# Optimization experiments

Measured on AMD Instinct MI355X. Metric: run time of the kernel, lower is better.

Reference implementation:

```python
import jax, jax.numpy as jnp
import numpy as np

B, M, N, L = 8, 384, 1536, 20  # batch, checks (detectors), error mechanisms, BP layers
ROW_W = 8  # check-node degree of sparse parity-check matrix H


def setup_inputs() -> dict:
    key = jax.random.key(0)
    ks = jax.random.split(key, 10)
    # Sparse binary check matrix: each row has exactly ROW_W ones (LDPC-like DEM).
    rng = np.random.default_rng(0)
    H_np = np.zeros((M, N), np.float32)
    for i in range(M):
        H_np[i, rng.choice(N, ROW_W, replace=False)] = 1.0
    H = jnp.asarray(H_np)
    llrs = jax.random.uniform(ks[0], (N,), minval=0.5, maxval=2.0)
    syndromes = jax.random.randint(ks[1], (B, M, 1), 0, 2).astype(jnp.float32)
    errors = jax.random.randint(ks[2], (B, N), 0, 2).astype(jnp.float32)
    # Per-layer learned weights (damped so 20 BP iterations stay numerically stable).
    weights_de = jax.random.uniform(ks[3], (L, M, N), minval=0.1, maxval=0.25)
    weights_llr = jax.random.uniform(ks[4], (L, N), minval=0.5, maxval=1.0)
    marg_weights_de = jax.random.uniform(ks[5], (M, N), minval=0.5, maxval=1.0)
    marg_weights_llr = jax.random.uniform(ks[6], (N,), minval=0.5, maxval=1.0)
    residual_weights = jax.random.uniform(ks[7], (L,), minval=0.0, maxval=0.1)
    rhos = jnp.ones((L,), jnp.float32) / L  # init: ones normalized by layers
    return dict(syndromes=syndromes, errors=errors, H=H, llrs=llrs,
                weights_de=weights_de, weights_llr=weights_llr,
                marg_weights_de=marg_weights_de, marg_weights_llr=marg_weights_llr,
                residual_weights=residual_weights, rhos=rhos)


def reference(syndromes, errors, H, llrs, weights_de, weights_llr,
              marg_weights_de, marg_weights_llr, residual_weights, rhos):
    sign = (1.0 - 2.0 * syndromes) * H          # (B,M,N): (-1)^syndrome masked by H
    one_minus_e = 1.0 - errors                  # (B,N)

    def step(msg_dn, per_layer):
        w_de, w_llr, res_w, rho = per_layer
        # --- error (variable) node update ---
        base = H * (llrs * w_llr)                                     # (M,N)
        msg_en = (base + jnp.sum(msg_dn * w_de, axis=1, keepdims=True)) * H - msg_dn
        # --- detector (check) node update: tanh-product with self-exclusion by division ---
        d = jnp.tanh(msg_en * 0.5)
        d = jnp.where(d == 0.0, 1.0, d)
        p = jnp.prod(d, axis=2, keepdims=True)                        # (B,M,1)
        msg_dn_new = 2.0 * jnp.arctanh(p / d) * sign + res_w * msg_dn
        # --- marginals (beliefs) + per-layer loss ---
        beliefs = jnp.sum(msg_dn_new * marg_weights_de, axis=1) + llrs * marg_weights_llr  # (B,N)
        loss_b = jnp.sum(jax.nn.softplus(beliefs) - one_minus_e * beliefs, axis=1) * rho   # (B,)
        return msg_dn_new, loss_b

    msg0 = jnp.zeros((syndromes.shape[0], H.shape[0], H.shape[1]), jnp.float32)
    _, losses = jax.lax.scan(step, msg0, (weights_de, weights_llr, residual_weights, rhos))
    return jnp.sum(losses) / syndromes.shape[0]  # scalar mean-over-batch loss
```

## Files before the change

### kernel.cpp

```cpp
#include <hip/hip_runtime.h>
#include <math.h>

#define MB 8
#define MM 384
#define NN 1536
#define LL 20
#define RW 8
#define HE 4
#define NE (MM*RW)
#define NT 768
#define VP 12
#define VG 3

#define LOG2E 1.44269504f
#define LN2   0.69314718f

#define SOFT_BAR() asm volatile("s_waitcnt lgkmcnt(0)\n\ts_barrier" ::: "memory")

static __device__ __forceinline__ float dpp_xor1(float x) {
    return __int_as_float(
        __builtin_amdgcn_mov_dpp(__float_as_int(x), 0xB1, 0xF, 0xF, true));
}

__global__ __launch_bounds__(256) void setup_kernel(
    const float* __restrict__ H,
    const float* __restrict__ llrs,
    const float* __restrict__ w_llr,
    const float* __restrict__ w_de,
    const float* __restrict__ marg_de,
    int*   __restrict__ col_pack,
    float* __restrict__ base_e,
    float* __restrict__ wde_vT,
    float* __restrict__ marg_vT,
    int*   __restrict__ gcnt,
    float* __restrict__ out) {
    const int m = blockIdx.x;
    const int t = threadIdx.x;
    const int w = t >> 6, lane = t & 63;
    __shared__ int s_qcol[4][RW];
    __shared__ int s_qcnt[4];
    __shared__ int s_col[RW];
    __shared__ int s_pos[RW];

    const float* row = H + (size_t)m * NN;
    int count = 0;
    for (int c0 = w * 384; c0 < (w + 1) * 384; c0 += 64) {
        float v = row[c0 + lane];
        unsigned long long mask = __ballot(v != 0.0f);
        if (v != 0.0f) {
            int pos = count + (int)__popcll(mask & ((1ull << lane) - 1ull));
            if (pos < RW) s_qcol[w][pos] = c0 + lane;
        }
        count += (int)__popcll(mask);
    }
    if (lane == 0) s_qcnt[w] = (count < RW) ? count : RW;
    __syncthreads();
    if (t == 0) {
        int off = 0;
        for (int q = 0; q < 4; ++q)
            for (int i = 0; i < s_qcnt[q]; ++i) {
                if (off < RW) s_col[off] = s_qcol[q][i];
                ++off;
            }
    }
    __syncthreads();

    if (t < RW) {
        int c = s_col[t];
        int pos = atomicAdd(&gcnt[c], 1);
        if (pos >= VP) pos = VP - 1;
        int ps = (pos & ~3) | ((pos & 3) ^ ((c >> 3) & 3));
        s_pos[t] = ps;
        col_pack[m * RW + t] = c | (ps << 16);
        marg_vT[((ps >> 2) * NN + c) * 4 + (ps & 3)] = marg_de[m * NN + c] * LN2;
    }
    if (m == 0 && t == 0) out[0] = 0.0f;
    __syncthreads();

    for (int idx = t; idx < LL * RW; idx += 256) {
        int l = idx >> 3;
        int k = idx & 7;
        int c = s_col[k];
        int ps = s_pos[k];
        wde_vT[((l * VG + (ps >> 2)) * NN + c) * 4 + (ps & 3)] =
            w_de[(size_t)l * MM * NN + (size_t)m * NN + c];
        base_e[l * NE + m * RW + k] = llrs[c] * w_llr[l * NN + c] * LOG2E;
    }
}

#define LAYER_BODY(lv, WC0, WC1, WN0, WN1, BN)                                \
{                                                                             \
      \
    {                                                                         \
        int lb = ((lv) + 1 < LL) ? ((lv) + 1) : (LL - 1);                     \
        _Pragma("unroll")                                                     \
        for (int jg = 0; jg < VG; ++jg) {                                     \
            float4 a = ((const float4*)wde_vT)[(lb * VG + jg) * NN + t];      \
            WN0[jg*4+0]=a.x; WN0[jg*4+1]=a.y; WN0[jg*4+2]=a.z; WN0[jg*4+3]=a.w; \
            float4 c4 = ((const float4*)wde_vT)[(lb * VG + jg) * NN + t + NT];\
            WN1[jg*4+0]=c4.x; WN1[jg*4+1]=c4.y; WN1[jg*4+2]=c4.z; WN1[jg*4+3]=c4.w; \
        }                                                                     \
        const float4 bp4 = ((const float4*)(base_e_g + lb * NE))[t];          \
        BN[0]=bp4.x; BN[1]=bp4.y; BN[2]=bp4.z; BN[3]=bp4.w;                   \
    }                                                                         \
                 \
    float4 g0a = ((const float4*)s_cN)[t];                                    \
    float4 g0b = ((const float4*)s_cN)[t + NT];                               \
    float belx0 = bias[0], belx1 = bias[1];                                   \
    {                                                                         \
        float S0 = g0a.x*WC0[0] + g0a.y*WC0[1] + g0a.z*WC0[2] + g0a.w*WC0[3]; \
        float S1 = g0b.x*WC1[0] + g0b.y*WC1[1] + g0b.z*WC1[2] + g0b.w*WC1[3]; \
        if (deg0 > 4) {                                                       \
            float4 a = ((const float4*)s_cN)[NN + t];                         \
            S0    += a.x*WC0[4] + a.y*WC0[5] + a.z*WC0[6] + a.w*WC0[7];       \
            belx0 += a.x*mg0[4] + a.y*mg0[5] + a.z*mg0[6] + a.w*mg0[7];       \
        }                                                                     \
        if (deg1 > 4) {                                                       \
            float4 c4 = ((const float4*)s_cN)[NN + t + NT];                   \
            S1    += c4.x*WC1[4] + c4.y*WC1[5] + c4.z*WC1[6] + c4.w*WC1[7];   \
            belx1 += c4.x*mg1[4] + c4.y*mg1[5] + c4.z*mg1[6] + c4.w*mg1[7];   \
        }                                                                     \
        if (deg0 > 8) {                                                       \
            float4 a = ((const float4*)s_cN)[2 * NN + t];                     \
            S0    += a.x*WC0[8] + a.y*WC0[9] + a.z*WC0[10] + a.w*WC0[11];     \
            belx0 += a.x*mg0[8] + a.y*mg0[9] + a.z*mg0[10] + a.w*mg0[11];     \
        }                                                                     \
        if (deg1 > 8) {                                                       \
            float4 c4 = ((const float4*)s_cN)[2 * NN + t + NT];               \
            S1    += c4.x*WC1[8] + c4.y*WC1[9] + c4.z*WC1[10] + c4.w*WC1[11]; \
            belx1 += c4.x*mg1[8] + c4.y*mg1[9] + c4.z*mg1[10] + c4.w*mg1[11]; \
        }                                                                     \
        s_S[t]      = S0;                                                     \
        s_S[t + NT] = S1;                                                     \
    }                                                                         \
    SOFT_BAR();      \
    {                                                                         \
                                     \
        float ss[HE];                                                         \
        _Pragma("unroll")                                                     \
        for (int k = 0; k < HE; ++k) ss[k] = s_S[col[k]];                     \
                            \
        if ((lv) > 0) {                                                       \
            const float rr = rhos[(lv) - 1];                                  \
            float bel0 = belx0 + g0a.x*mg0[0] + g0a.y*mg0[1]                  \
                               + g0a.z*mg0[2] + g0a.w*mg0[3];                 \
            float bel1 = belx1 + g0b.x*mg1[0] + g0b.y*mg1[1]                  \
                               + g0b.z*mg1[2] + g0b.w*mg1[3];                 \
            float sp0 = fmaxf(bel0, 0.0f) + __logf(1.0f + __expf(-fabsf(bel0))); \
            float sp1 = fmaxf(bel1, 0.0f) + __logf(1.0f + __expf(-fabsf(bel1))); \
            loss += rr * ((sp0 - omeg[0] * bel0) + (sp1 - omeg[1] * bel1));   \
        }                                                                     \
        const float rw_ = res_w[(lv)];                                        \
        float d[HE];                                                          \
        _Pragma("unroll")                                                     \
        for (int k = 0; k < HE; ++k) {                                        \
            float te = tm[k] + ss[k];                        \
            float e  = __builtin_amdgcn_exp2f(te);                            \
            float dd = 1.0f - 2.0f * __builtin_amdgcn_rcpf(e + 1.0f);         \
            dd = fminf(fmaxf(dd, -1.0f), 1.0f);                               \
            if (dd == 0.0f) dd = 1.0f;                                        \
            d[k] = dd;                                                        \
        }                                                                     \
        float pre2 = d[0] * d[1];                                             \
        float suf1 = d[2] * d[3];                                             \
        float p4   = pre2 * suf1;                                             \
        float pot  = dpp_xor1(p4);                                            \
        float ex[HE];                                                         \
        ex[0] = d[1] * suf1;                                                  \
        ex[1] = d[0] * suf1;                                                  \
        ex[2] = pre2 * d[3];                                                  \
        ex[3] = pre2 * d[2];                                                  \
        _Pragma("unroll")                                                     \
        for (int k = 0; k < HE; ++k) {                                        \
            float x  = ex[k] * pot;                                           \
            float la = __builtin_amdgcn_logf(1.0f + x);                       \
            float lb2 = __builtin_amdgcn_logf(1.0f - x);                      \
            float nm = sgn * (la - lb2) + rw_ * msg[k];      \
            msg[k] = nm;                                                      \
            s_cN[esl[k]] = nm;                                                \
        }                                                                     \
                        \
        _Pragma("unroll")                                                     \
        for (int k = 0; k < HE; ++k) tm[k] = BN[k] - msg[k];                  \
    }                                                                         \
    SOFT_BAR();                  \
}

__global__ __launch_bounds__(NT) void bp_kernel(
    const float* __restrict__ synd,
    const float* __restrict__ errors,
    const float* __restrict__ llrs,
    const float* __restrict__ marg_llr,
    const float* __restrict__ res_w,
    const float* __restrict__ rhos,
    const int*   __restrict__ col_pack,
    const float* __restrict__ base_e_g,
    const float* __restrict__ wde_vT,
    const float* __restrict__ marg_vT,
    const int*   __restrict__ gdeg,
    float* __restrict__ out) {

    __shared__ float s_cN[NN * VP];
    __shared__ float s_S[NN];
    __shared__ float s_red[12];

    const int b = blockIdx.x;
    const int t = threadIdx.x;
    const int m = t >> 1;

    int col[HE], esl[HE];
    {
        const int4 cp = ((const int4*)col_pack)[t];
        int v[HE] = {cp.x, cp.y, cp.z, cp.w};
        #pragma unroll
        for (int k = 0; k < HE; ++k) {
            int c = v[k] & 0xFFFF, pos = v[k] >> 16;
            col[k] = c;
            esl[k] = ((pos >> 2) * NN + c) * 4 + (pos & 3);
        }
    }
    float msg[HE] = {0.0f, 0.0f, 0.0f, 0.0f};
    const float sgn = 1.0f - 2.0f * synd[b * MM + m];

    const int deg0 = gdeg[t];
    const int deg1 = gdeg[t + NT];
    float bias[2], omeg[2];
    #pragma unroll
    for (int i = 0; i < 2; ++i) {
        int n = t + i * NT;
        bias[i] = llrs[n] * marg_llr[n];
        omeg[i] = 1.0f - errors[b * NN + n];
    }

    float mg0[VP], mg1[VP];
    #pragma unroll
    for (int jg = 0; jg < VG; ++jg) {
        float4 a = ((const float4*)marg_vT)[jg * NN + t];
        mg0[jg*4+0] = a.x; mg0[jg*4+1] = a.y; mg0[jg*4+2] = a.z; mg0[jg*4+3] = a.w;
        float4 c4 = ((const float4*)marg_vT)[jg * NN + t + NT];
        mg1[jg*4+0] = c4.x; mg1[jg*4+1] = c4.y; mg1[jg*4+2] = c4.z; mg1[jg*4+3] = c4.w;
    }
    float wcA0[VP], wcA1[VP], wcB0[VP], wcB1[VP];
    #pragma unroll
    for (int jg = 0; jg < VG; ++jg) {
        float4 a = ((const float4*)wde_vT)[jg * NN + t];
        wcA0[jg*4+0] = a.x; wcA0[jg*4+1] = a.y; wcA0[jg*4+2] = a.z; wcA0[jg*4+3] = a.w;
        float4 c4 = ((const float4*)wde_vT)[jg * NN + t + NT];
        wcA1[jg*4+0] = c4.x; wcA1[jg*4+1] = c4.y; wcA1[jg*4+2] = c4.z; wcA1[jg*4+3] = c4.w;
    }
    float bcA[HE], bcB[HE];
    float tm[HE];
    {
        const float4 bp4 = ((const float4*)base_e_g)[t];
        bcA[0] = bp4.x; bcA[1] = bp4.y; bcA[2] = bp4.z; bcA[3] = bp4.w;
        #pragma unroll
        for (int k = 0; k < HE; ++k) tm[k] = bcA[k];
    }

    #pragma unroll
    for (int j = 0; j < 6; ++j)
        ((float4*)s_cN)[j * NT + t] = make_float4(0.f, 0.f, 0.f, 0.f);

    float loss = 0.0f;
    __syncthreads();

    for (int l = 0; l < LL; l += 2) {
        LAYER_BODY(l,     wcA0, wcA1, wcB0, wcB1, bcB);
        LAYER_BODY(l + 1, wcB0, wcB1, wcA0, wcA1, bcA);
    }

    {
        const float rr = rhos[LL - 1];
        float bel0 = bias[0], bel1 = bias[1];
        {
            float4 a = ((const float4*)s_cN)[t];
            bel0 += a.x*mg0[0] + a.y*mg0[1] + a.z*mg0[2] + a.w*mg0[3];
            float4 c4 = ((const float4*)s_cN)[t + NT];
            bel1 += c4.x*mg1[0] + c4.y*mg1[1] + c4.z*mg1[2] + c4.w*mg1[3];
        }
        if (deg0 > 4) {
            float4 a = ((const float4*)s_cN)[NN + t];
            bel0 += a.x*mg0[4] + a.y*mg0[5] + a.z*mg0[6] + a.w*mg0[7];
        }
        if (deg1 > 4) {
            float4 c4 = ((const float4*)s_cN)[NN + t + NT];
            bel1 += c4.x*mg1[4] + c4.y*mg1[5] + c4.z*mg1[6] + c4.w*mg1[7];
        }
        if (deg0 > 8) {
            float4 a = ((const float4*)s_cN)[2 * NN + t];
            bel0 += a.x*mg0[8] + a.y*mg0[9] + a.z*mg0[10] + a.w*mg0[11];
        }
        if (deg1 > 8) {
            float4 c4 = ((const float4*)s_cN)[2 * NN + t + NT];
            bel1 += c4.x*mg1[8] + c4.y*mg1[9] + c4.z*mg1[10] + c4.w*mg1[11];
        }
        float sp0 = fmaxf(bel0, 0.0f) + __logf(1.0f + __expf(-fabsf(bel0)));
        float sp1 = fmaxf(bel1, 0.0f) + __logf(1.0f + __expf(-fabsf(bel1)));
        loss += rr * ((sp0 - omeg[0] * bel0) + (sp1 - omeg[1] * bel1));
    }

    #pragma unroll
    for (int off = 32; off > 0; off >>= 1)
        loss += __shfl_down(loss, off, 64);
    int wave = t >> 6, lane = t & 63;
    if (lane == 0) s_red[wave] = loss;
    __syncthreads();
    if (t == 0) {
        float tot = 0.0f;
        #pragma unroll
        for (int w = 0; w < 12; ++w) tot += s_red[w];
        atomicAdd(out, tot * (1.0f / (float)MB));
    }
}

extern "C" void kernel_launch(void* const* d_in, const int* in_sizes, int n_in,
                              void* d_out, int out_size, void* d_ws, size_t ws_size,
                              hipStream_t stream) {
    const float* synd     = (const float*)d_in[0];
    const float* errors   = (const float*)d_in[1];
    const float* H        = (const float*)d_in[2];
    const float* llrs     = (const float*)d_in[3];
    const float* w_de     = (const float*)d_in[4];
    const float* w_llr    = (const float*)d_in[5];
    const float* marg_de  = (const float*)d_in[6];
    const float* marg_llr = (const float*)d_in[7];
    const float* res_w    = (const float*)d_in[8];
    const float* rhos     = (const float*)d_in[9];
    float* out = (float*)d_out;

    float* wde_vT  = (float*)d_ws;
    float* marg_vT = wde_vT + (size_t)LL * VG * NN * 4;
    int*   gcnt    = (int*)(marg_vT + VG * NN * 4);
    float* base_e  = (float*)(gcnt + NN);
    int*   col_pack= (int*)(base_e + (size_t)LL * NE);

    hipMemsetAsync(gcnt, 0, NN * sizeof(int), stream);
    setup_kernel<<<MM, 256, 0, stream>>>(H, llrs, w_llr, w_de, marg_de,
                                         col_pack, base_e, wde_vT, marg_vT,
                                         gcnt, out);
    bp_kernel<<<MB, NT, 0, stream>>>(synd, errors, llrs, marg_llr, res_w, rhos,
                                     col_pack, base_e, wde_vT, marg_vT, gcnt, out);
}
```

Before: 142.2 us.

## Process two batch elements per workgroup and simplify extrinsic tanh-product via logs

Each workgroup now decodes two batch samples at once, halving the grid from 8 to 4 blocks. The per-layer weight loads, barriers and column metadata are shared across both samples, and the two independent dependency chains can interleave. The extrinsic check message is now computed as log|d+P| - log|d-P| from the full product, replacing the per-edge leave-one-out products. This trades parallelism across CUs for more instruction-level parallelism, double the LDS use and more registers per thread, which could lower occupancy or lengthen the critical path.

```diff
diff --git a/kernel.cpp b/kernel.cpp
--- a/kernel.cpp
+++ b/kernel.cpp
@@ -90,7 +90,7 @@
 
 #define LAYER_BODY(lv, WC0, WC1, WN0, WN1, BN)                                \
 {                                                                             \
-      \
+            \
     {                                                                         \
         int lb = ((lv) + 1 < LL) ? ((lv) + 1) : (LL - 1);                     \
         _Pragma("unroll")                                                     \
@@ -103,85 +103,121 @@
         const float4 bp4 = ((const float4*)(base_e_g + lb * NE))[t];          \
         BN[0]=bp4.x; BN[1]=bp4.y; BN[2]=bp4.z; BN[3]=bp4.w;                   \
     }                                                                         \
-                 \
-    float4 g0a = ((const float4*)s_cN)[t];                                    \
-    float4 g0b = ((const float4*)s_cN)[t + NT];                               \
-    float belx0 = bias[0], belx1 = bias[1];                                   \
+         \
+    float bel00, bel01, bel10, bel11;                                         \
     {                                                                         \
-        float S0 = g0a.x*WC0[0] + g0a.y*WC0[1] + g0a.z*WC0[2] + g0a.w*WC0[3]; \
-        float S1 = g0b.x*WC1[0] + g0b.y*WC1[1] + g0b.z*WC1[2] + g0b.w*WC1[3]; \
+        float4 xa0 = ((const float4*)s_cN0)[t];                               \
+        float4 xb0 = ((const float4*)s_cN0)[t + NT];                          \
+        float4 xa1 = ((const float4*)s_cN1)[t];                               \
+        float4 xb1 = ((const float4*)s_cN1)[t + NT];                          \
+        float S00 = xa0.x*WC0[0] + xa0.y*WC0[1] + xa0.z*WC0[2] + xa0.w*WC0[3]; \
+        float S01 = xb0.x*WC1[0] + xb0.y*WC1[1] + xb0.z*WC1[2] + xb0.w*WC1[3]; \
+        float S10 = xa1.x*WC0[0] + xa1.y*WC0[1] + xa1.z*WC0[2] + xa1.w*WC0[3]; \
+        float S11 = xb1.x*WC1[0] + xb1.y*WC1[1] + xb1.z*WC1[2] + xb1.w*WC1[3]; \
+        bel00 = bias[0] + xa0.x*mg0[0] + xa0.y*mg0[1] + xa0.z*mg0[2] + xa0.w*mg0[3]; \
+        bel01 = bias[1] + xb0.x*mg1[0] + xb0.y*mg1[1] + xb0.z*mg1[2] + xb0.w*mg1[3]; \
+        bel10 = bias[0] + xa1.x*mg0[0] + xa1.y*mg0[1] + xa1.z*mg0[2] + xa1.w*mg0[3]; \
+        bel11 = bias[1] + xb1.x*mg1[0] + xb1.y*mg1[1] + xb1.z*mg1[2] + xb1.w*mg1[3]; \
         if (deg0 > 4) {                                                       \
-            float4 a = ((const float4*)s_cN)[NN + t];                         \
-            S0    += a.x*WC0[4] + a.y*WC0[5] + a.z*WC0[6] + a.w*WC0[7];       \
-            belx0 += a.x*mg0[4] + a.y*mg0[5] + a.z*mg0[6] + a.w*mg0[7];       \
+            float4 a = ((const float4*)s_cN0)[NN + t];                        \
+            float4 c4 = ((const float4*)s_cN1)[NN + t];                       \
+            S00   += a.x*WC0[4] + a.y*WC0[5] + a.z*WC0[6] + a.w*WC0[7];       \
+            bel00 += a.x*mg0[4] + a.y*mg0[5] + a.z*mg0[6] + a.w*mg0[7];       \
+            S10   += c4.x*WC0[4] + c4.y*WC0[5] + c4.z*WC0[6] + c4.w*WC0[7];   \
+            bel10 += c4.x*mg0[4] + c4.y*mg0[5] + c4.z*mg0[6] + c4.w*mg0[7];   \
         }                                                                     \
         if (deg1 > 4) {                                                       \
-            float4 c4 = ((const float4*)s_cN)[NN + t + NT];                   \
-            S1    += c4.x*WC1[4] + c4.y*WC1[5] + c4.z*WC1[6] + c4.w*WC1[7];   \
-            belx1 += c4.x*mg1[4] + c4.y*mg1[5] + c4.z*mg1[6] + c4.w*mg1[7];   \
+            float4 a = ((const float4*)s_cN0)[NN + t + NT];                   \
+            float4 c4 = ((const float4*)s_cN1)[NN + t + NT];                  \
+            S01   += a.x*WC1[4] + a.y*WC1[5] + a.z*WC1[6] + a.w*WC1[7];       \
+            bel01 += a.x*mg1[4] + a.y*mg1[5] + a.z*mg1[6] + a.w*mg1[7];       \
+            S11   += c4.x*WC1[4] + c4.y*WC1[5] + c4.z*WC1[6] + c4.w*WC1[7];   \
+            bel11 += c4.x*mg1[4] + c4.y*mg1[5] + c4.z*mg1[6] + c4.w*mg1[7];   \
         }                                                                     \
         if (deg0 > 8) {                                                       \
-            float4 a = ((const float4*)s_cN)[2 * NN + t];                     \
-            S0    += a.x*WC0[8] + a.y*WC0[9] + a.z*WC0[10] + a.w*WC0[11];     \
-            belx0 += a.x*mg0[8] + a.y*mg0[9] + a.z*mg0[10] + a.w*mg0[11];     \
+            float4 a = ((const float4*)s_cN0)[2 * NN + t];                    \
+            float4 c4 = ((const float4*)s_cN1)[2 * NN + t];                   \
+            S00   += a.x*WC0[8] + a.y*WC0[9] + a.z*WC0[10] + a.w*WC0[11];     \
+            bel00 += a.x*mg0[8] + a.y*mg0[9] + a.z*mg0[10] + a.w*mg0[11];     \
+            S10   += c4.x*WC0[8] + c4.y*WC0[9] + c4.z*WC0[10] + c4.w*WC0[11]; \
+            bel10 += c4.x*mg0[8] + c4.y*mg0[9] + c4.z*mg0[10] + c4.w*mg0[11]; \
         }                                                                     \
         if (deg1 > 8) {                                                       \
-            float4 c4 = ((const float4*)s_cN)[2 * NN + t + NT];               \
-            S1    += c4.x*WC1[8] + c4.y*WC1[9] + c4.z*WC1[10] + c4.w*WC1[11]; \
-            belx1 += c4.x*mg1[8] + c4.y*mg1[9] + c4.z*mg1[10] + c4.w*mg1[11]; \
-        }                                                                     \
-        s_S[t]      = S0;                                                     \
-        s_S[t + NT] = S1;                                                     \
+            float4 a = ((const float4*)s_cN0)[2 * NN + t + NT];               \
+            float4 c4 = ((const float4*)s_cN1)[2 * NN + t + NT];              \
+            S01   += a.x*WC1[8] + a.y*WC1[9] + a.z*WC1[10] + a.w*WC1[11];     \
+            bel01 += a.x*mg1[8] + a.y*mg1[9] + a.z*mg1[10] + a.w*mg1[11];     \
+            S11   += c4.x*WC1[8] + c4.y*WC1[9] + c4.z*WC1[10] + c4.w*WC1[11]; \
+            bel11 += c4.x*mg1[8] + c4.y*mg1[9] + c4.z*mg1[10] + c4.w*mg1[11]; \
+        }                                                                     \
+        s_S0[t]      = S00;                                                   \
+        s_S0[t + NT] = S01;                                                   \
+        s_S1[t]      = S10;                                                   \
+        s_S1[t + NT] = S11;                                                   \
     }                                                                         \
-    SOFT_BAR();      \
+    SOFT_BAR();                \
     {                                                                         \
-                                     \
-        float ss[HE];                                                         \
-        _Pragma("unroll")                                                     \
-        for (int k = 0; k < HE; ++k) ss[k] = s_S[col[k]];                     \
-                            \
+                      \
+        float ss0[HE], ss1[HE];                                               \
+        _Pragma("unroll")                                                     \
+        for (int k = 0; k < HE; ++k) ss0[k] = s_S0[col[k]];                   \
+        _Pragma("unroll")                                                     \
+        for (int k = 0; k < HE; ++k) ss1[k] = s_S1[col[k]];                   \
+                               \
         if ((lv) > 0) {                                                       \
             const float rr = rhos[(lv) - 1];                                  \
-            float bel0 = belx0 + g0a.x*mg0[0] + g0a.y*mg0[1]                  \
-                               + g0a.z*mg0[2] + g0a.w*mg0[3];                 \
-            float bel1 = belx1 + g0b.x*mg1[0] + g0b.y*mg1[1]                  \
-                               + g0b.z*mg1[2] + g0b.w*mg1[3];                 \
-            float sp0 = fmaxf(bel0, 0.0f) + __logf(1.0f + __expf(-fabsf(bel0))); \
-            float sp1 = fmaxf(bel1, 0.0f) + __logf(1.0f + __expf(-fabsf(bel1))); \
-            loss += rr * ((sp0 - omeg[0] * bel0) + (sp1 - omeg[1] * bel1));   \
+            float sp00 = fmaxf(bel00, 0.0f) + __logf(1.0f + __expf(-fabsf(bel00))); \
+            float sp01 = fmaxf(bel01, 0.0f) + __logf(1.0f + __expf(-fabsf(bel01))); \
+            float sp10 = fmaxf(bel10, 0.0f) + __logf(1.0f + __expf(-fabsf(bel10))); \
+            float sp11 = fmaxf(bel11, 0.0f) + __logf(1.0f + __expf(-fabsf(bel11))); \
+            loss += rr * ((sp00 - omeg0[0] * bel00) + (sp01 - omeg0[1] * bel01) \
+                        + (sp10 - omeg1[0] * bel10) + (sp11 - omeg1[1] * bel11)); \
         }                                                                     \
         const float rw_ = res_w[(lv)];                                        \
-        float d[HE];                                                          \
+        float d0_[HE], d1_[HE];                                               \
         _Pragma("unroll")                                                     \
         for (int k = 0; k < HE; ++k) {                                        \
-            float te = tm[k] + ss[k];                        \
+            float te = tm0[k] + ss0[k];                      \
             float e  = __builtin_amdgcn_exp2f(te);                            \
             float dd = 1.0f - 2.0f * __builtin_amdgcn_rcpf(e + 1.0f);         \
             dd = fminf(fmaxf(dd, -1.0f), 1.0f);                               \
             if (dd == 0.0f) dd = 1.0f;                                        \
-            d[k] = dd;                                                        \
-        }                                                                     \
-        float pre2 = d[0] * d[1];                                             \
-        float suf1 = d[2] * d[3];                                             \
-        float p4   = pre2 * suf1;                                             \
-        float pot  = dpp_xor1(p4);                                            \
-        float ex[HE];                                                         \
-        ex[0] = d[1] * suf1;                                                  \
-        ex[1] = d[0] * suf1;                                                  \
-        ex[2] = pre2 * d[3];                                                  \
-        ex[3] = pre2 * d[2];                                                  \
+            d0_[k] = dd;                                                      \
+        }                                                                     \
         _Pragma("unroll")                                                     \
         for (int k = 0; k < HE; ++k) {                                        \
-            float x  = ex[k] * pot;                                           \
-            float la = __builtin_amdgcn_logf(1.0f + x);                       \
-            float lb2 = __builtin_amdgcn_logf(1.0f - x);                      \
-            float nm = sgn * (la - lb2) + rw_ * msg[k];      \
-            msg[k] = nm;                                                      \
-            s_cN[esl[k]] = nm;                                                \
+            float te = tm1[k] + ss1[k];                                       \
+            float e  = __builtin_amdgcn_exp2f(te);                            \
+            float dd = 1.0f - 2.0f * __builtin_amdgcn_rcpf(e + 1.0f);         \
+            dd = fminf(fmaxf(dd, -1.0f), 1.0f);                               \
+            if (dd == 0.0f) dd = 1.0f;                                        \
+            d1_[k] = dd;                                                      \
+        }                                                                     \
+        float P0 = (d0_[0] * d0_[1]) * (d0_[2] * d0_[3]);                     \
+        float P1 = (d1_[0] * d1_[1]) * (d1_[2] * d1_[3]);                     \
+        P0 *= dpp_xor1(P0);                      \
+        P1 *= dpp_xor1(P1);                                                   \
+        _Pragma("unroll")                                                     \
+        for (int k = 0; k < HE; ++k) {                                        \
+                  \
+            float la = __builtin_amdgcn_logf(fabsf(d0_[k] + P0));             \
+            float lb2 = __builtin_amdgcn_logf(fabsf(d0_[k] - P0));            \
+            float nm = sgn0 * (la - lb2) + rw_ * msg0[k];       \
+            msg0[k] = nm;                                                     \
+            s_cN0[esl[k]] = nm;                                               \
+        }                                                                     \
+        _Pragma("unroll")                                                     \
+        for (int k = 0; k < HE; ++k) {                                        \
+            float la = __builtin_amdgcn_logf(fabsf(d1_[k] + P1));             \
+            float lb2 = __builtin_amdgcn_logf(fabsf(d1_[k] - P1));            \
+            float nm = sgn1 * (la - lb2) + rw_ * msg1[k];                     \
+            msg1[k] = nm;                                                     \
+            s_cN1[esl[k]] = nm;                                               \
         }                                                                     \
                         \
         _Pragma("unroll")                                                     \
-        for (int k = 0; k < HE; ++k) tm[k] = BN[k] - msg[k];                  \
+        for (int k = 0; k < HE; ++k) { tm0[k] = BN[k] - msg0[k];              \
+                                       tm1[k] = BN[k] - msg1[k]; }            \
     }                                                                         \
     SOFT_BAR();                  \
 }
@@ -200,11 +236,14 @@
     const int*   __restrict__ gdeg,
     float* __restrict__ out) {
 
-    __shared__ float s_cN[NN * VP];
-    __shared__ float s_S[NN];
+    __shared__ float s_cN0[NN * VP];
+    __shared__ float s_cN1[NN * VP];
+    __shared__ float s_S0[NN];
+    __shared__ float s_S1[NN];
     __shared__ float s_red[12];
 
-    const int b = blockIdx.x;
+    const int b0 = blockIdx.x;
+    const int b1 = blockIdx.x + MB / 2;
     const int t = threadIdx.x;
     const int m = t >> 1;
 
@@ -219,17 +258,20 @@
             esl[k] = ((pos >> 2) * NN + c) * 4 + (pos & 3);
         }
     }
-    float msg[HE] = {0.0f, 0.0f, 0.0f, 0.0f};
-    const float sgn = 1.0f - 2.0f * synd[b * MM + m];
+    float msg0[HE] = {0.0f, 0.0f, 0.0f, 0.0f};
+    float msg1[HE] = {0.0f, 0.0f, 0.0f, 0.0f};
+    const float sgn0 = 1.0f - 2.0f * synd[b0 * MM + m];
+    const float sgn1 = 1.0f - 2.0f * synd[b1 * MM + m];
 
     const int deg0 = gdeg[t];
     const int deg1 = gdeg[t + NT];
-    float bias[2], omeg[2];
+    float bias[2], omeg0[2], omeg1[2];
     #pragma unroll
     for (int i = 0; i < 2; ++i) {
         int n = t + i * NT;
         bias[i] = llrs[n] * marg_llr[n];
-        omeg[i] = 1.0f - errors[b * NN + n];
+        omeg0[i] = 1.0f - errors[b0 * NN + n];
+        omeg1[i] = 1.0f - errors[b1 * NN + n];
     }
 
     float mg0[VP], mg1[VP];
@@ -249,17 +291,19 @@
         wcA1[jg*4+0] = c4.x; wcA1[jg*4+1] = c4.y; wcA1[jg*4+2] = c4.z; wcA1[jg*4+3] = c4.w;
     }
     float bcA[HE], bcB[HE];
-    float tm[HE];
+    float tm0[HE], tm1[HE];
     {
         const float4 bp4 = ((const float4*)base_e_g)[t];
         bcA[0] = bp4.x; bcA[1] = bp4.y; bcA[2] = bp4.z; bcA[3] = bp4.w;
         #pragma unroll
-        for (int k = 0; k < HE; ++k) tm[k] = bcA[k];
+        for (int k = 0; k < HE; ++k) { tm0[k] = bcA[k]; tm1[k] = bcA[k]; }
     }
 
     #pragma unroll
-    for (int j = 0; j < 6; ++j)
-        ((float4*)s_cN)[j * NT + t] = make_float4(0.f, 0.f, 0.f, 0.f);
+    for (int j = 0; j < 6; ++j) {
+        ((float4*)s_cN0)[j * NT + t] = make_float4(0.f, 0.f, 0.f, 0.f);
+        ((float4*)s_cN1)[j * NT + t] = make_float4(0.f, 0.f, 0.f, 0.f);
+    }
 
     float loss = 0.0f;
     __syncthreads();
@@ -271,32 +315,47 @@
 
     {
         const float rr = rhos[LL - 1];
-        float bel0 = bias[0], bel1 = bias[1];
+        float bel00 = bias[0], bel01 = bias[1], bel10 = bias[0], bel11 = bias[1];
         {
-            float4 a = ((const float4*)s_cN)[t];
-            bel0 += a.x*mg0[0] + a.y*mg0[1] + a.z*mg0[2] + a.w*mg0[3];
-            float4 c4 = ((const float4*)s_cN)[t + NT];
-            bel1 += c4.x*mg1[0] + c4.y*mg1[1] + c4.z*mg1[2] + c4.w*mg1[3];
+            float4 a = ((const float4*)s_cN0)[t];
+            float4 c4 = ((const float4*)s_cN0)[t + NT];
+            bel00 += a.x*mg0[0] + a.y*mg0[1] + a.z*mg0[2] + a.w*mg0[3];
+            bel01 += c4.x*mg1[0] + c4.y*mg1[1] + c4.z*mg1[2] + c4.w*mg1[3];
+            float4 a1 = ((const float4*)s_cN1)[t];
+            float4 c41 = ((const float4*)s_cN1)[t + NT];
+            bel10 += a1.x*mg0[0] + a1.y*mg0[1] + a1.z*mg0[2] + a1.w*mg0[3];
+            bel11 += c41.x*mg1[0] + c41.y*mg1[1] + c41.z*mg1[2] + c41.w*mg1[3];
         }
         if (deg0 > 4) {
-            float4 a = ((const float4*)s_cN)[NN + t];
-            bel0 += a.x*mg0[4] + a.y*mg0[5] + a.z*mg0[6] + a.w*mg0[7];
+            float4 a = ((const float4*)s_cN0)[NN + t];
+            float4 c4 = ((const float4*)s_cN1)[NN + t];
+            bel00 += a.x*mg0[4] + a.y*mg0[5] + a.z*mg0[6] + a.w*mg0[7];
+            bel10 += c4.x*mg0[4] + c4.y*mg0[5] + c4.z*mg0[6] + c4.w*mg0[7];
         }
         if (deg1 > 4) {
-            float4 c4 = ((const float4*)s_cN)[NN + t + NT];
-            bel1 += c4.x*mg1[4] + c4.y*mg1[5] + c4.z*mg1[6] + c4.w*mg1[7];
+            float4 a = ((const float4*)s_cN0)[NN + t + NT];
+            float4 c4 = ((const float4*)s_cN1)[NN + t + NT];
+            bel01 += a.x*mg1[4] + a.y*mg1[5] + a.z*mg1[6] + a.w*mg1[7];
+            bel11 += c4.x*mg1[4] + c4.y*mg1[5] + c4.z*mg1[6] + c4.w*mg1[7];
         }
         if (deg0 > 8) {
-            float4 a = ((const float4*)s_cN)[2 * NN + t];
-            bel0 += a.x*mg0[8] + a.y*mg0[9] + a.z*mg0[10] + a.w*mg0[11];
+            float4 a = ((const float4*)s_cN0)[2 * NN + t];
+            float4 c4 = ((const float4*)s_cN1)[2 * NN + t];
+            bel00 += a.x*mg0[8] + a.y*mg0[9] + a.z*mg0[10] + a.w*mg0[11];
+            bel10 += c4.x*mg0[8] + c4.y*mg0[9] + c4.z*mg0[10] + c4.w*mg0[11];
         }
         if (deg1 > 8) {
-            float4 c4 = ((const float4*)s_cN)[2 * NN + t + NT];
-            bel1 += c4.x*mg1[8] + c4.y*mg1[9] + c4.z*mg1[10] + c4.w*mg1[11];
-        }
-        float sp0 = fmaxf(bel0, 0.0f) + __logf(1.0f + __expf(-fabsf(bel0)));
-        float sp1 = fmaxf(bel1, 0.0f) + __logf(1.0f + __expf(-fabsf(bel1)));
-        loss += rr * ((sp0 - omeg[0] * bel0) + (sp1 - omeg[1] * bel1));
+            float4 a = ((const float4*)s_cN0)[2 * NN + t + NT];
+            float4 c4 = ((const float4*)s_cN1)[2 * NN + t + NT];
+            bel01 += a.x*mg1[8] + a.y*mg1[9] + a.z*mg1[10] + a.w*mg1[11];
+            bel11 += c4.x*mg1[8] + c4.y*mg1[9] + c4.z*mg1[10] + c4.w*mg1[11];
+        }
+        float sp00 = fmaxf(bel00, 0.0f) + __logf(1.0f + __expf(-fabsf(bel00)));
+        float sp01 = fmaxf(bel01, 0.0f) + __logf(1.0f + __expf(-fabsf(bel01)));
+        float sp10 = fmaxf(bel10, 0.0f) + __logf(1.0f + __expf(-fabsf(bel10)));
+        float sp11 = fmaxf(bel11, 0.0f) + __logf(1.0f + __expf(-fabsf(bel11)));
+        loss += rr * ((sp00 - omeg0[0] * bel00) + (sp01 - omeg0[1] * bel01)
+                    + (sp10 - omeg1[0] * bel10) + (sp11 - omeg1[1] * bel11));
     }
 
     #pragma unroll
@@ -338,6 +397,7 @@
     setup_kernel<<<MM, 256, 0, stream>>>(H, llrs, w_llr, w_de, marg_de,
                                          col_pack, base_e, wde_vT, marg_vT,
                                          gcnt, out);
-    bp_kernel<<<MB, NT, 0, stream>>>(synd, errors, llrs, marg_llr, res_w, rhos,
-                                     col_pack, base_e, wde_vT, marg_vT, gcnt, out);
+    bp_kernel<<<MB / 2, NT, 0, stream>>>(synd, errors, llrs, marg_llr, res_w,
+                                         rhos, col_pack, base_e, wde_vT,
+                                         marg_vT, gcnt, out);
 }
```

Measured after the change: 155.1 us. +9.1%, slower.

## Scatter variable sums to per-edge LDS slots and simplify extrinsic product math

Applied to the files above, without the earlier changes.

The setup kernel now records, for each column and slot, the edge index that maps to it. The variable-node phase scatters each column's sum S into every edge slot it feeds, using a dump region for unused slots. The check phase can then read its four sums with one vectorized float4 load instead of four gathered loads. The extrinsic log-ratio is rewritten as log|d+P| - log|d-P| using the full row product, which removes the per-edge exclusion products. The cost is extra LDS scatter stores, more registers for the index arrays, and possible precision loss when d and P are nearly equal.

```diff
diff --git a/kernel.cpp b/kernel.cpp
--- a/kernel.cpp
+++ b/kernel.cpp
@@ -33,6 +33,7 @@
     float* __restrict__ wde_vT,
     float* __restrict__ marg_vT,
     int*   __restrict__ gcnt,
+    int*   __restrict__ cse,
     float* __restrict__ out) {
     const int m = blockIdx.x;
     const int t = threadIdx.x;
@@ -69,6 +70,7 @@
         int c = s_col[t];
         int pos = atomicAdd(&gcnt[c], 1);
         if (pos >= VP) pos = VP - 1;
+        cse[c * VP + pos] = m * RW + t;
         int ps = (pos & ~3) | ((pos & 3) ^ ((c >> 3) & 3));
         s_pos[t] = ps;
         col_pack[m * RW + t] = c | (ps << 16);
@@ -130,15 +132,24 @@
             S1    += c4.x*WC1[8] + c4.y*WC1[9] + c4.z*WC1[10] + c4.w*WC1[11]; \
             belx1 += c4.x*mg1[8] + c4.y*mg1[9] + c4.z*mg1[10] + c4.w*mg1[11]; \
         }                                                                     \
-        s_S[t]      = S0;                                                     \
-        s_S[t + NT] = S1;                                                     \
+            \
+        s_Se[ce0[0]] = S0; s_Se[ce0[1]] = S0;                                 \
+        s_Se[ce0[2]] = S0; s_Se[ce0[3]] = S0;                                 \
+        s_Se[ce1[0]] = S1; s_Se[ce1[1]] = S1;                                 \
+        s_Se[ce1[2]] = S1; s_Se[ce1[3]] = S1;                                 \
+        if (deg0 > 4) { s_Se[ce0[4]] = S0; s_Se[ce0[5]] = S0;                 \
+                        s_Se[ce0[6]] = S0; s_Se[ce0[7]] = S0; }               \
+        if (deg1 > 4) { s_Se[ce1[4]] = S1; s_Se[ce1[5]] = S1;                 \
+                        s_Se[ce1[6]] = S1; s_Se[ce1[7]] = S1; }               \
+        if (deg0 > 8) { s_Se[ce0[8]] = S0; s_Se[ce0[9]] = S0;                 \
+                        s_Se[ce0[10]] = S0; s_Se[ce0[11]] = S0; }             \
+        if (deg1 > 8) { s_Se[ce1[8]] = S1; s_Se[ce1[9]] = S1;                 \
+                        s_Se[ce1[10]] = S1; s_Se[ce1[11]] = S1; }             \
     }                                                                         \
-    SOFT_BAR();      \
+    SOFT_BAR();     \
     {                                                                         \
-                                     \
-        float ss[HE];                                                         \
-        _Pragma("unroll")                                                     \
-        for (int k = 0; k < HE; ++k) ss[k] = s_S[col[k]];                     \
+                \
+        const float4 ssv = ((const float4*)s_Se)[t];                          \
                             \
         if ((lv) > 0) {                                                       \
             const float rr = rhos[(lv) - 1];                                  \
@@ -151,6 +162,7 @@
             loss += rr * ((sp0 - omeg[0] * bel0) + (sp1 - omeg[1] * bel1));   \
         }                                                                     \
         const float rw_ = res_w[(lv)];                                        \
+        float ss[HE] = {ssv.x, ssv.y, ssv.z, ssv.w};                          \
         float d[HE];                                                          \
         _Pragma("unroll")                                                     \
         for (int k = 0; k < HE; ++k) {                                        \
@@ -161,20 +173,13 @@
             if (dd == 0.0f) dd = 1.0f;                                        \
             d[k] = dd;                                                        \
         }                                                                     \
-        float pre2 = d[0] * d[1];                                             \
-        float suf1 = d[2] * d[3];                                             \
-        float p4   = pre2 * suf1;                                             \
-        float pot  = dpp_xor1(p4);                                            \
-        float ex[HE];                                                         \
-        ex[0] = d[1] * suf1;                                                  \
-        ex[1] = d[0] * suf1;                                                  \
-        ex[2] = pre2 * d[3];                                                  \
-        ex[3] = pre2 * d[2];                                                  \
+        float p4 = (d[0] * d[1]) * (d[2] * d[3]);                             \
+        float P  = p4 * dpp_xor1(p4);            \
         _Pragma("unroll")                                                     \
         for (int k = 0; k < HE; ++k) {                                        \
-            float x  = ex[k] * pot;                                           \
-            float la = __builtin_amdgcn_logf(1.0f + x);                       \
-            float lb2 = __builtin_amdgcn_logf(1.0f - x);                      \
+              \
+            float la  = __builtin_amdgcn_logf(fabsf(d[k] + P));               \
+            float lb2 = __builtin_amdgcn_logf(fabsf(d[k] - P));               \
             float nm = sgn * (la - lb2) + rw_ * msg[k];      \
             msg[k] = nm;                                                      \
             s_cN[esl[k]] = nm;                                                \
@@ -198,10 +203,11 @@
     const float* __restrict__ wde_vT,
     const float* __restrict__ marg_vT,
     const int*   __restrict__ gdeg,
+    const int*   __restrict__ cse,
     float* __restrict__ out) {
 
     __shared__ float s_cN[NN * VP];
-    __shared__ float s_S[NN];
+    __shared__ __align__(16) float s_Se[NE + 64];
     __shared__ float s_red[12];
 
     const int b = blockIdx.x;
@@ -230,6 +236,25 @@
         int n = t + i * NT;
         bias[i] = llrs[n] * marg_llr[n];
         omeg[i] = 1.0f - errors[b * NN + n];
+    }
+
+    int ce0[VP], ce1[VP];
+    {
+        const int4* cb0 = (const int4*)(cse + (size_t)t * VP);
+        const int4* cb1 = (const int4*)(cse + (size_t)(t + NT) * VP);
+        int4 g;
+        g = cb0[0]; ce0[0]=g.x; ce0[1]=g.y; ce0[2]=g.z; ce0[3]=g.w;
+        g = cb0[1]; ce0[4]=g.x; ce0[5]=g.y; ce0[6]=g.z; ce0[7]=g.w;
+        g = cb0[2]; ce0[8]=g.x; ce0[9]=g.y; ce0[10]=g.z; ce0[11]=g.w;
+        g = cb1[0]; ce1[0]=g.x; ce1[1]=g.y; ce1[2]=g.z; ce1[3]=g.w;
+        g = cb1[1]; ce1[4]=g.x; ce1[5]=g.y; ce1[6]=g.z; ce1[7]=g.w;
+        g = cb1[2]; ce1[8]=g.x; ce1[9]=g.y; ce1[10]=g.z; ce1[11]=g.w;
+        const int dump = NE + (t & 63);
+        #pragma unroll
+        for (int j = 0; j < VP; ++j) {
+            ce0[j] = (j < deg0) ? ce0[j] : dump;
+            ce1[j] = (j < deg1) ? ce1[j] : dump;
+        }
     }
 
     float mg0[VP], mg1[VP];
@@ -333,11 +358,13 @@
     int*   gcnt    = (int*)(marg_vT + VG * NN * 4);
     float* base_e  = (float*)(gcnt + NN);
     int*   col_pack= (int*)(base_e + (size_t)LL * NE);
+    int*   cse     = (int*)(col_pack + NE);
 
     hipMemsetAsync(gcnt, 0, NN * sizeof(int), stream);
     setup_kernel<<<MM, 256, 0, stream>>>(H, llrs, w_llr, w_de, marg_de,
                                          col_pack, base_e, wde_vT, marg_vT,
-                                         gcnt, out);
+                                         gcnt, cse, out);
     bp_kernel<<<MB, NT, 0, stream>>>(synd, errors, llrs, marg_llr, res_w, rhos,
-                                     col_pack, base_e, wde_vT, marg_vT, gcnt, out);
-}
+                                     col_pack, base_e, wde_vT, marg_vT, gcnt,
+                                     cse, out);
+}
```

Measured after the change: 146.3 us. 2.9% more time.

## Pre-weight edge messages at the check side and simplify exclusion arctanh math

Applied to the files above, without the earlier changes.

The de weights and marginal weights are now applied per edge by the check-side thread, which writes two weighted copies (s_cW, s_cM) to shared memory. Variable-side sums then become plain adds instead of FMAs against per-variable weight registers. The self-excluded arctanh is computed as log|d+P| - log|d-P| from the full product, which removes the prefix/suffix products. This lowers register pressure and global weight traffic (edge-indexed rather than variable-transposed). In exchange it doubles shared-memory footprint and LDS writes, and the division-free identity can lose precision when d is small.

```diff
diff --git a/kernel.cpp b/kernel.cpp
--- a/kernel.cpp
+++ b/kernel.cpp
@@ -30,8 +30,8 @@
     const float* __restrict__ marg_de,
     int*   __restrict__ col_pack,
     float* __restrict__ base_e,
-    float* __restrict__ wde_vT,
-    float* __restrict__ marg_vT,
+    float* __restrict__ wde_e,
+    float* __restrict__ marg_e,
     int*   __restrict__ gcnt,
     float* __restrict__ out) {
     const int m = blockIdx.x;
@@ -40,7 +40,6 @@
     __shared__ int s_qcol[4][RW];
     __shared__ int s_qcnt[4];
     __shared__ int s_col[RW];
-    __shared__ int s_pos[RW];
 
     const float* row = H + (size_t)m * NN;
     int count = 0;
@@ -70,9 +69,8 @@
         int pos = atomicAdd(&gcnt[c], 1);
         if (pos >= VP) pos = VP - 1;
         int ps = (pos & ~3) | ((pos & 3) ^ ((c >> 3) & 3));
-        s_pos[t] = ps;
         col_pack[m * RW + t] = c | (ps << 16);
-        marg_vT[((ps >> 2) * NN + c) * 4 + (ps & 3)] = marg_de[m * NN + c] * LN2;
+        marg_e[m * RW + t] = marg_de[m * NN + c] * LN2;
     }
     if (m == 0 && t == 0) out[0] = 0.0f;
     __syncthreads();
@@ -81,59 +79,59 @@
         int l = idx >> 3;
         int k = idx & 7;
         int c = s_col[k];
-        int ps = s_pos[k];
-        wde_vT[((l * VG + (ps >> 2)) * NN + c) * 4 + (ps & 3)] =
-            w_de[(size_t)l * MM * NN + (size_t)m * NN + c];
+        wde_e[l * NE + m * RW + k] = w_de[(size_t)l * MM * NN + (size_t)m * NN + c];
         base_e[l * NE + m * RW + k] = llrs[c] * w_llr[l * NN + c] * LOG2E;
     }
 }
 
-#define LAYER_BODY(lv, WC0, WC1, WN0, WN1, BN)                                \
+#define LAYER_BODY(lv, WNC, WNN, BN)                                          \
 {                                                                             \
-      \
+                 \
     {                                                                         \
+        int la2 = ((lv) + 2 < LL) ? ((lv) + 2) : (LL - 1);                    \
+        const float4 w4 = ((const float4*)(wde_e_g + la2 * NE))[t];           \
+        WNN[0]=w4.x; WNN[1]=w4.y; WNN[2]=w4.z; WNN[3]=w4.w;                   \
         int lb = ((lv) + 1 < LL) ? ((lv) + 1) : (LL - 1);                     \
-        _Pragma("unroll")                                                     \
-        for (int jg = 0; jg < VG; ++jg) {                                     \
-            float4 a = ((const float4*)wde_vT)[(lb * VG + jg) * NN + t];      \
-            WN0[jg*4+0]=a.x; WN0[jg*4+1]=a.y; WN0[jg*4+2]=a.z; WN0[jg*4+3]=a.w; \
-            float4 c4 = ((const float4*)wde_vT)[(lb * VG + jg) * NN + t + NT];\
-            WN1[jg*4+0]=c4.x; WN1[jg*4+1]=c4.y; WN1[jg*4+2]=c4.z; WN1[jg*4+3]=c4.w; \
-        }                                                                     \
         const float4 bp4 = ((const float4*)(base_e_g + lb * NE))[t];          \
         BN[0]=bp4.x; BN[1]=bp4.y; BN[2]=bp4.z; BN[3]=bp4.w;                   \
     }                                                                         \
-                 \
-    float4 g0a = ((const float4*)s_cN)[t];                                    \
-    float4 g0b = ((const float4*)s_cN)[t + NT];                               \
+          \
+    float4 m0a = ((const float4*)s_cM)[t];                                    \
+    float4 m0b = ((const float4*)s_cM)[t + NT];                               \
     float belx0 = bias[0], belx1 = bias[1];                                   \
     {                                                                         \
-        float S0 = g0a.x*WC0[0] + g0a.y*WC0[1] + g0a.z*WC0[2] + g0a.w*WC0[3]; \
-        float S1 = g0b.x*WC1[0] + g0b.y*WC1[1] + g0b.z*WC1[2] + g0b.w*WC1[3]; \
+        float4 w0a = ((const float4*)s_cW)[t];                                \
+        float4 w0b = ((const float4*)s_cW)[t + NT];                           \
+        float S0 = (w0a.x + w0a.y) + (w0a.z + w0a.w);                         \
+        float S1 = (w0b.x + w0b.y) + (w0b.z + w0b.w);                         \
         if (deg0 > 4) {                                                       \
-            float4 a = ((const float4*)s_cN)[NN + t];                         \
-            S0    += a.x*WC0[4] + a.y*WC0[5] + a.z*WC0[6] + a.w*WC0[7];       \
-            belx0 += a.x*mg0[4] + a.y*mg0[5] + a.z*mg0[6] + a.w*mg0[7];       \
+            float4 a = ((const float4*)s_cW)[NN + t];                         \
+            float4 q = ((const float4*)s_cM)[NN + t];                         \
+            S0    += (a.x + a.y) + (a.z + a.w);                               \
+            belx0 += (q.x + q.y) + (q.z + q.w);                               \
         }                                                                     \
         if (deg1 > 4) {                                                       \
-            float4 c4 = ((const float4*)s_cN)[NN + t + NT];                   \
-            S1    += c4.x*WC1[4] + c4.y*WC1[5] + c4.z*WC1[6] + c4.w*WC1[7];   \
-            belx1 += c4.x*mg1[4] + c4.y*mg1[5] + c4.z*mg1[6] + c4.w*mg1[7];   \
+            float4 a = ((const float4*)s_cW)[NN + t + NT];                    \
+            float4 q = ((const float4*)s_cM)[NN + t + NT];                    \
+            S1    += (a.x + a.y) + (a.z + a.w);                               \
+            belx1 += (q.x + q.y) + (q.z + q.w);                               \
         }                                                                     \
         if (deg0 > 8) {                                                       \
-            float4 a = ((const float4*)s_cN)[2 * NN + t];                     \
-            S0    += a.x*WC0[8] + a.y*WC0[9] + a.z*WC0[10] + a.w*WC0[11];     \
-            belx0 += a.x*mg0[8] + a.y*mg0[9] + a.z*mg0[10] + a.w*mg0[11];     \
+            float4 a = ((const float4*)s_cW)[2 * NN + t];                     \
+            float4 q = ((const float4*)s_cM)[2 * NN + t];                     \
+            S0    += (a.x + a.y) + (a.z + a.w);                               \
+            belx0 += (q.x + q.y) + (q.z + q.w);                               \
         }                                                                     \
         if (deg1 > 8) {                                                       \
-            float4 c4 = ((const float4*)s_cN)[2 * NN + t + NT];               \
-            S1    += c4.x*WC1[8] + c4.y*WC1[9] + c4.z*WC1[10] + c4.w*WC1[11]; \
-            belx1 += c4.x*mg1[8] + c4.y*mg1[9] + c4.z*mg1[10] + c4.w*mg1[11]; \
+            float4 a = ((const float4*)s_cW)[2 * NN + t + NT];                \
+            float4 q = ((const float4*)s_cM)[2 * NN + t + NT];                \
+            S1    += (a.x + a.y) + (a.z + a.w);                               \
+            belx1 += (q.x + q.y) + (q.z + q.w);                               \
         }                                                                     \
         s_S[t]      = S0;                                                     \
         s_S[t + NT] = S1;                                                     \
     }                                                                         \
-    SOFT_BAR();      \
+    SOFT_BAR();           \
     {                                                                         \
                                      \
         float ss[HE];                                                         \
@@ -142,10 +140,8 @@
                             \
         if ((lv) > 0) {                                                       \
             const float rr = rhos[(lv) - 1];                                  \
-            float bel0 = belx0 + g0a.x*mg0[0] + g0a.y*mg0[1]                  \
-                               + g0a.z*mg0[2] + g0a.w*mg0[3];                 \
-            float bel1 = belx1 + g0b.x*mg1[0] + g0b.y*mg1[1]                  \
-                               + g0b.z*mg1[2] + g0b.w*mg1[3];                 \
+            float bel0 = belx0 + (m0a.x + m0a.y) + (m0a.z + m0a.w);           \
+            float bel1 = belx1 + (m0b.x + m0b.y) + (m0b.z + m0b.w);           \
             float sp0 = fmaxf(bel0, 0.0f) + __logf(1.0f + __expf(-fabsf(bel0))); \
             float sp1 = fmaxf(bel1, 0.0f) + __logf(1.0f + __expf(-fabsf(bel1))); \
             loss += rr * ((sp0 - omeg[0] * bel0) + (sp1 - omeg[1] * bel1));   \
@@ -161,29 +157,23 @@
             if (dd == 0.0f) dd = 1.0f;                                        \
             d[k] = dd;                                                        \
         }                                                                     \
-        float pre2 = d[0] * d[1];                                             \
-        float suf1 = d[2] * d[3];                                             \
-        float p4   = pre2 * suf1;                                             \
-        float pot  = dpp_xor1(p4);                                            \
-        float ex[HE];                                                         \
-        ex[0] = d[1] * suf1;                                                  \
-        ex[1] = d[0] * suf1;                                                  \
-        ex[2] = pre2 * d[3];                                                  \
-        ex[3] = pre2 * d[2];                                                  \
+        float p4 = (d[0] * d[1]) * (d[2] * d[3]);                             \
+        float P  = p4 * dpp_xor1(p4);            \
         _Pragma("unroll")                                                     \
         for (int k = 0; k < HE; ++k) {                                        \
-            float x  = ex[k] * pot;                                           \
-            float la = __builtin_amdgcn_logf(1.0f + x);                       \
-            float lb2 = __builtin_amdgcn_logf(1.0f - x);                      \
+              \
+            float la  = __builtin_amdgcn_logf(fabsf(d[k] + P));               \
+            float lb2 = __builtin_amdgcn_logf(fabsf(d[k] - P));               \
             float nm = sgn * (la - lb2) + rw_ * msg[k];      \
             msg[k] = nm;                                                      \
-            s_cN[esl[k]] = nm;                                                \
+            s_cW[esl[k]] = nm * WNC[k];          \
+            s_cM[esl[k]] = nm * me[k];          \
         }                                                                     \
                         \
         _Pragma("unroll")                                                     \
         for (int k = 0; k < HE; ++k) tm[k] = BN[k] - msg[k];                  \
     }                                                                         \
-    SOFT_BAR();                  \
+    SOFT_BAR();             \
 }
 
 __global__ __launch_bounds__(NT) void bp_kernel(
@@ -195,12 +185,13 @@
     const float* __restrict__ rhos,
     const int*   __restrict__ col_pack,
     const float* __restrict__ base_e_g,
-    const float* __restrict__ wde_vT,
-    const float* __restrict__ marg_vT,
+    const float* __restrict__ wde_e_g,
+    const float* __restrict__ marg_e_g,
     const int*   __restrict__ gdeg,
     float* __restrict__ out) {
 
-    __shared__ float s_cN[NN * VP];
+    __shared__ float s_cW[NN * VP];
+    __shared__ float s_cM[NN * VP];
     __shared__ float s_S[NN];
     __shared__ float s_red[12];
 
@@ -232,21 +223,15 @@
         omeg[i] = 1.0f - errors[b * NN + n];
     }
 
-    float mg0[VP], mg1[VP];
-    #pragma unroll
-    for (int jg = 0; jg < VG; ++jg) {
-        float4 a = ((const float4*)marg_vT)[jg * NN + t];
-        mg0[jg*4+0] = a.x; mg0[jg*4+1] = a.y; mg0[jg*4+2] = a.z; mg0[jg*4+3] = a.w;
-        float4 c4 = ((const float4*)marg_vT)[jg * NN + t + NT];
-        mg1[jg*4+0] = c4.x; mg1[jg*4+1] = c4.y; mg1[jg*4+2] = c4.z; mg1[jg*4+3] = c4.w;
-    }
-    float wcA0[VP], wcA1[VP], wcB0[VP], wcB1[VP];
-    #pragma unroll
-    for (int jg = 0; jg < VG; ++jg) {
-        float4 a = ((const float4*)wde_vT)[jg * NN + t];
-        wcA0[jg*4+0] = a.x; wcA0[jg*4+1] = a.y; wcA0[jg*4+2] = a.z; wcA0[jg*4+3] = a.w;
-        float4 c4 = ((const float4*)wde_vT)[jg * NN + t + NT];
-        wcA1[jg*4+0] = c4.x; wcA1[jg*4+1] = c4.y; wcA1[jg*4+2] = c4.z; wcA1[jg*4+3] = c4.w;
+    float me[HE];
+    {
+        const float4 m4 = ((const float4*)marg_e_g)[t];
+        me[0] = m4.x; me[1] = m4.y; me[2] = m4.z; me[3] = m4.w;
+    }
+    float wnA[HE], wnB[HE];
+    {
+        const float4 w4 = ((const float4*)(wde_e_g + NE))[t];
+        wnA[0] = w4.x; wnA[1] = w4.y; wnA[2] = w4.z; wnA[3] = w4.w;
     }
     float bcA[HE], bcB[HE];
     float tm[HE];
@@ -258,41 +243,43 @@
     }
 
     #pragma unroll
-    for (int j = 0; j < 6; ++j)
-        ((float4*)s_cN)[j * NT + t] = make_float4(0.f, 0.f, 0.f, 0.f);
+    for (int j = 0; j < 6; ++j) {
+        ((float4*)s_cW)[j * NT + t] = make_float4(0.f, 0.f, 0.f, 0.f);
+        ((float4*)s_cM)[j * NT + t] = make_float4(0.f, 0.f, 0.f, 0.f);
+    }
 
     float loss = 0.0f;
     __syncthreads();
 
     for (int l = 0; l < LL; l += 2) {
-        LAYER_BODY(l,     wcA0, wcA1, wcB0, wcB1, bcB);
-        LAYER_BODY(l + 1, wcB0, wcB1, wcA0, wcA1, bcA);
+        LAYER_BODY(l,     wnA, wnB, bcB);
+        LAYER_BODY(l + 1, wnB, wnA, bcA);
     }
 
     {
         const float rr = rhos[LL - 1];
         float bel0 = bias[0], bel1 = bias[1];
         {
-            float4 a = ((const float4*)s_cN)[t];
-            bel0 += a.x*mg0[0] + a.y*mg0[1] + a.z*mg0[2] + a.w*mg0[3];
-            float4 c4 = ((const float4*)s_cN)[t + NT];
-            bel1 += c4.x*mg1[0] + c4.y*mg1[1] + c4.z*mg1[2] + c4.w*mg1[3];
+            float4 a = ((const float4*)s_cM)[t];
+            float4 c4 = ((const float4*)s_cM)[t + NT];
+            bel0 += (a.x + a.y) + (a.z + a.w);
+            bel1 += (c4.x + c4.y) + (c4.z + c4.w);
         }
         if (deg0 > 4) {
-            float4 a = ((const float4*)s_cN)[NN + t];
-            bel0 += a.x*mg0[4] + a.y*mg0[5] + a.z*mg0[6] + a.w*mg0[7];
+            float4 a = ((const float4*)s_cM)[NN + t];
+            bel0 += (a.x + a.y) + (a.z + a.w);
         }
         if (deg1 > 4) {
-            float4 c4 = ((const float4*)s_cN)[NN + t + NT];
-            bel1 += c4.x*mg1[4] + c4.y*mg1[5] + c4.z*mg1[6] + c4.w*mg1[7];
+            float4 c4 = ((const float4*)s_cM)[NN + t + NT];
+            bel1 += (c4.x + c4.y) + (c4.z + c4.w);
         }
         if (deg0 > 8) {
-            float4 a = ((const float4*)s_cN)[2 * NN + t];
-            bel0 += a.x*mg0[8] + a.y*mg0[9] + a.z*mg0[10] + a.w*mg0[11];
+            float4 a = ((const float4*)s_cM)[2 * NN + t];
+            bel0 += (a.x + a.y) + (a.z + a.w);
         }
         if (deg1 > 8) {
-            float4 c4 = ((const float4*)s_cN)[2 * NN + t + NT];
-            bel1 += c4.x*mg1[8] + c4.y*mg1[9] + c4.z*mg1[10] + c4.w*mg1[11];
+            float4 c4 = ((const float4*)s_cM)[2 * NN + t + NT];
+            bel1 += (c4.x + c4.y) + (c4.z + c4.w);
         }
         float sp0 = fmaxf(bel0, 0.0f) + __logf(1.0f + __expf(-fabsf(bel0)));
         float sp1 = fmaxf(bel1, 0.0f) + __logf(1.0f + __expf(-fabsf(bel1)));
@@ -328,16 +315,16 @@
     const float* rhos     = (const float*)d_in[9];
     float* out = (float*)d_out;
 
-    float* wde_vT  = (float*)d_ws;
-    float* marg_vT = wde_vT + (size_t)LL * VG * NN * 4;
-    int*   gcnt    = (int*)(marg_vT + VG * NN * 4);
-    float* base_e  = (float*)(gcnt + NN);
-    int*   col_pack= (int*)(base_e + (size_t)LL * NE);
+    float* wde_e   = (float*)d_ws;
+    float* base_e  = wde_e + (size_t)LL * NE;
+    float* marg_e  = base_e + (size_t)LL * NE;
+    int*   gcnt    = (int*)(marg_e + NE);
+    int*   col_pack= (int*)(gcnt + NN);
 
     hipMemsetAsync(gcnt, 0, NN * sizeof(int), stream);
     setup_kernel<<<MM, 256, 0, stream>>>(H, llrs, w_llr, w_de, marg_de,
-                                         col_pack, base_e, wde_vT, marg_vT,
+                                         col_pack, base_e, wde_e, marg_e,
                                          gcnt, out);
     bp_kernel<<<MB, NT, 0, stream>>>(synd, errors, llrs, marg_llr, res_w, rhos,
-                                     col_pack, base_e, wde_vT, marg_vT, gcnt, out);
-}
+                                     col_pack, base_e, wde_e, marg_e, gcnt, out);
+}
```

Result: faster. 131.9 us, median of 2 (-7.2%).
